# Performance work log

Hardware: AMD Instinct MI355X
Metric: run time of the kernel (lower is better)

## Reference

```python
import jax, jax.numpy as jnp
import numpy as np

BS, QS, H, NH, HD = 2, 2048, 1024, 16, 64


def setup_inputs() -> dict:
    key = jax.random.key(0)
    ks = jax.random.split(key, 10)
    s = 0.02
    x = jax.random.normal(ks[0], (BS, QS, H), jnp.float32)
    pos_emb = jax.random.normal(ks[1], (QS, H), jnp.float32)
    rr_bias = jax.random.normal(ks[2], (NH, HD), jnp.float32) * s
    rw_bias = jax.random.normal(ks[3], (NH, HD), jnp.float32) * s
    Wq = jax.random.normal(ks[4], (H, NH * HD), jnp.float32) * s
    Wk = jax.random.normal(ks[5], (H, NH * HD), jnp.float32) * s
    Wv = jax.random.normal(ks[6], (H, NH * HD), jnp.float32) * s
    Wr = jax.random.normal(ks[7], (H, NH * HD), jnp.float32) * s
    Wo = jax.random.normal(ks[8], (NH * HD, H), jnp.float32) * s
    ln_gamma = jnp.ones((H,), jnp.float32)
    ln_beta = jnp.zeros((H,), jnp.float32)
    # True = masked (filled with -inf); strict causal mask, ms = ks - qs = 0
    mask = jnp.triu(jnp.ones((QS, QS), bool), 1)
    return {"x": x, "mask": mask, "pos_emb": pos_emb, "rr_bias": rr_bias,
            "rw_bias": rw_bias, "Wq": Wq, "Wk": Wk, "Wv": Wv, "Wr": Wr,
            "Wo": Wo, "ln_gamma": ln_gamma, "ln_beta": ln_beta}


def _left_shift(x, bs):
    # x: [bs, qs, ks, n_head] -- Transformer-XL relative-shift trick
    b, qs, ksz, nh = x.shape
    pad = jnp.zeros((b, qs, 1, nh), x.dtype)
    xp = jnp.concatenate([pad, x], axis=2).reshape(b, ksz + 1, qs, nh)
    x = xp[:, 1:].reshape(b, qs, ksz, nh)
    # NOTE: original code uses diagonal offset (ks - bs) with bs = batch size
    tri = jnp.tril(jnp.ones((qs, ksz), x.dtype), ksz - bs)
    return x * tri[None, :, :, None]


def reference(x, mask, pos_emb, rr_bias, rw_bias, Wq, Wk, Wv, Wr, Wo, ln_gamma, ln_beta):
    bs, qs, hid = x.shape
    nh, dh = rr_bias.shape
    ksz = qs  # self-attention, no memory
    scale = 1.0 / dh ** 0.5
    q = (x @ Wq).reshape(bs, qs, nh, dh)
    k = (x @ Wk).reshape(bs, ksz, nh, dh)
    v = (x @ Wv).reshape(bs, ksz, nh, dh)
    r = (pos_emb @ Wr).reshape(qs, nh, dh)
    AC = jnp.einsum('bqnd,bknd->bqkn', q + rw_bias[None, None], k)
    BD = jnp.einsum('bqnd,knd->bqkn', q + rr_bias[None, None], r)
    BD = _left_shift(BD, bs)
    score = (AC + BD) * scale
    score = jnp.where(mask[None, :, :, None], -jnp.inf, score)
    prob = jax.nn.softmax(score, axis=2)  # softmax over key axis
    att = jnp.einsum('bqkn,bknd->bqnd', prob, v)
    out = att.reshape(bs, qs, nh * dh) @ Wo
    out = x + out  # residual (post-lnorm variant)
    mu = out.mean(-1, keepdims=True)
    var = ((out - mu) ** 2).mean(-1, keepdims=True)
    return (out - mu) / jnp.sqrt(var + 1e-5) * ln_gamma + ln_beta
```

## Files before the change

### kernel.cpp

```cpp
#include <hip/hip_runtime.h>
#include <hip/hip_bf16.h>


typedef _Float16 f16;
typedef __attribute__((ext_vector_type(8))) _Float16 f16x8;
typedef __attribute__((ext_vector_type(4))) float f32x4;

__device__ __forceinline__ void gload16(const f16* g, f16* l) {
  __builtin_amdgcn_global_load_lds((__attribute__((address_space(1))) void*)(g),
                                   (__attribute__((address_space(3))) void*)(l), 16, 0, 0);
}

__global__ __launch_bounds__(256) void cast2_kernel(const float* __restrict__ a,
                                                    f16* __restrict__ ao, int na4,
                                                    const float* __restrict__ b,
                                                    f16* __restrict__ bo, int nb4) {
  int i = blockIdx.x * 256 + threadIdx.x;
  const float* src;
  f16* dst;
  int j;
  if (i < na4) { src = a; dst = ao; j = i; }
  else { j = i - na4; if (j >= nb4) return; src = b; dst = bo; }
  f32x4 v = *(const f32x4*)&src[j * 4];
  f16 o0 = (f16)v[0], o1 = (f16)v[1], o2 = (f16)v[2], o3 = (f16)v[3];
  f16* p = &dst[j * 4];
  p[0] = o0; p[1] = o1; p[2] = o2; p[3] = o3;
}

__global__ __launch_bounds__(256) void wtrans5_kernel(
    const float* __restrict__ W0, const float* __restrict__ W1, const float* __restrict__ W2,
    const float* __restrict__ W3, const float* __restrict__ W4,
    f16* __restrict__ T0, f16* __restrict__ T1, f16* __restrict__ T2,
    f16* __restrict__ T3, f16* __restrict__ T4) {
  __shared__ float tile[32][33];
  const float* W;
  f16* WT;
  switch (blockIdx.z) {
    case 0: W = W0; WT = T0; break;
    case 1: W = W1; WT = T1; break;
    case 2: W = W2; WT = T2; break;
    case 3: W = W3; WT = T3; break;
    default: W = W4; WT = T4; break;
  }
  int k0 = blockIdx.x * 32, n0 = blockIdx.y * 32;
  int tx = threadIdx.x, ty = threadIdx.y;
#pragma unroll
  for (int i = 0; i < 4; ++i)
    tile[ty + i * 8][tx] = W[(size_t)(k0 + ty + i * 8) * 1024 + n0 + tx];
  __syncthreads();
#pragma unroll
  for (int i = 0; i < 4; ++i)
    WT[(size_t)(n0 + ty + i * 8) * 1024 + k0 + tx] = (f16)tile[tx][ty + i * 8];
}

__global__ __launch_bounds__(256) void gemm_qkv(
    const f16* __restrict__ A, const f16* __restrict__ Bq, const f16* __restrict__ Bk,
    const f16* __restrict__ Bv, f16* __restrict__ Qw, f16* __restrict__ Qr,
    f16* __restrict__ Kb, f16* __restrict__ VTb,
    const float* __restrict__ rw, const float* __restrict__ rr) {
  __shared__ f16 sm[17408];
  f16* As = sm;
  f16* Bs = sm + 8192;
  const int bsel = blockIdx.x >> 3;
  const f16* Bw = bsel == 0 ? Bq : (bsel == 1 ? Bk : Bv);
  const int n0 = (blockIdx.x & 7) * 128, m0 = blockIdx.y * 128;
  const int tid = threadIdx.x, lane = tid & 63, wv = tid >> 6;
  const int wm = wv >> 1, wn = wv & 1, lg = lane >> 4, ln = lane & 15;
  const int srow = lane >> 3, scol = (lane & 7) * 8;
  f32x4 acc[4][4] = {};

  for (int kt = 0; kt < 16; ++kt) {
    __syncthreads();
#pragma unroll
    for (int i = 0; i < 4; ++i) {
      int c = wv * 4 + i;
      gload16(A + (size_t)(m0 + c * 8 + srow) * 1024 + kt * 64 + scol, &As[c * 512]);
      gload16(Bw + (size_t)(n0 + c * 8 + srow) * 1024 + kt * 64 + scol, &Bs[c * 512]);
    }
    __syncthreads();
#pragma unroll
    for (int ks = 0; ks < 2; ++ks) {
      f16x8 af[4], bfr[4];
#pragma unroll
      for (int mi = 0; mi < 4; ++mi)
        af[mi] = *(const f16x8*)&As[(wm * 64 + mi * 16 + ln) * 64 + ks * 32 + 8 * lg];
#pragma unroll
      for (int ni = 0; ni < 4; ++ni)
        bfr[ni] = *(const f16x8*)&Bs[(wn * 64 + ni * 16 + ln) * 64 + ks * 32 + 8 * lg];
#pragma unroll
      for (int mi = 0; mi < 4; ++mi)
#pragma unroll
        for (int ni = 0; ni < 4; ++ni)
          acc[mi][ni] = __builtin_amdgcn_mfma_f32_16x16x32_f16(af[mi], bfr[ni],
                                                               acc[mi][ni], 0, 0, 0);
    }
  }

  if (bsel == 2) {
    __syncthreads();
    f16* T = sm;
#pragma unroll
    for (int mi = 0; mi < 4; ++mi)
#pragma unroll
      for (int ni = 0; ni < 4; ++ni)
#pragma unroll
        for (int r = 0; r < 4; ++r) {
          int ml = wm * 64 + mi * 16 + 4 * lg + r;
          int cl = wn * 64 + ni * 16 + ln;
          T[cl * 136 + ml] = (f16)acc[mi][ni][r];
        }
    __syncthreads();
    int cl = tid >> 1, mb = (tid & 1) * 64;
    int gc = n0 + cl, gm = m0 + mb;
    int hh = gc >> 6, dd = gc & 63, bb = gm >> 11, ss = gm & 2047;
    f16* dst = VTb + ((size_t)(bb * 16 + hh) * 64 + dd) * 2048 + ss;
    const f16* srcT = &T[cl * 136 + mb];
#pragma unroll
    for (int i = 0; i < 8; ++i) *(f16x8*)&dst[i * 8] = *(const f16x8*)&srcT[i * 8];
  } else {
#pragma unroll
    for (int mi = 0; mi < 4; ++mi)
#pragma unroll
      for (int ni = 0; ni < 4; ++ni)
#pragma unroll
        for (int r = 0; r < 4; ++r) {
          int m = m0 + wm * 64 + mi * 16 + 4 * lg + r;
          int c = n0 + wn * 64 + ni * 16 + ln;
          float v = acc[mi][ni][r];
          size_t off = (size_t)m * 1024 + c;
          if (bsel == 0) {
            Qw[off] = (f16)(v + rw[c]);
            Qr[off] = (f16)(v + rr[c]);
          } else {
            Kb[off] = (f16)v;
          }
        }
  }
}

template <int MODE>
__global__ __launch_bounds__(256) void gemm64(
    const f16* __restrict__ A, const f16* __restrict__ Bw,
    f16* __restrict__ out0, float* __restrict__ fout, const float* __restrict__ xres) {
  __shared__ f16 As[4096];
  __shared__ f16 Bs[8192];
  const int tid = threadIdx.x, lane = tid & 63, wv = tid >> 6;
  const int wm = wv >> 1, wn = wv & 1, lg = lane >> 4, ln = lane & 15;
  const int m0 = blockIdx.y * 64, n0 = blockIdx.x * 128;
  const int srow = lane >> 3, scol = (lane & 7) * 8;
  f32x4 acc[2][4] = {};

  for (int kt = 0; kt < 16; ++kt) {
    __syncthreads();
#pragma unroll
    for (int i = 0; i < 2; ++i) {
      int c = wv * 2 + i;
      gload16(A + (size_t)(m0 + c * 8 + srow) * 1024 + kt * 64 + scol, &As[c * 512]);
    }
#pragma unroll
    for (int i = 0; i < 4; ++i) {
      int c = wv * 4 + i;
      gload16(Bw + (size_t)(n0 + c * 8 + srow) * 1024 + kt * 64 + scol, &Bs[c * 512]);
    }
    __syncthreads();
#pragma unroll
    for (int ks = 0; ks < 2; ++ks) {
      f16x8 af[2], bfr[4];
#pragma unroll
      for (int mi = 0; mi < 2; ++mi)
        af[mi] = *(const f16x8*)&As[(wm * 32 + mi * 16 + ln) * 64 + ks * 32 + 8 * lg];
#pragma unroll
      for (int ni = 0; ni < 4; ++ni)
        bfr[ni] = *(const f16x8*)&Bs[(wn * 64 + ni * 16 + ln) * 64 + ks * 32 + 8 * lg];
#pragma unroll
      for (int mi = 0; mi < 2; ++mi)
#pragma unroll
        for (int ni = 0; ni < 4; ++ni)
          acc[mi][ni] = __builtin_amdgcn_mfma_f32_16x16x32_f16(af[mi], bfr[ni],
                                                               acc[mi][ni], 0, 0, 0);
    }
  }
#pragma unroll
  for (int mi = 0; mi < 2; ++mi)
#pragma unroll
    for (int ni = 0; ni < 4; ++ni)
#pragma unroll
      for (int r = 0; r < 4; ++r) {
        int m = m0 + wm * 32 + mi * 16 + 4 * lg + r;
        int c = n0 + wn * 64 + ni * 16 + ln;
        size_t off = (size_t)m * 1024 + c;
        if (MODE == 3) out0[off] = (f16)acc[mi][ni][r];
        else fout[off] = acc[mi][ni][r] + xres[off];
      }
}

__device__ __forceinline__ void chunk_map(int c, int& qt, int& ci) {
  if (c < 8) { qt = c; ci = 0; }
  else if (c < 24) { qt = 8 + ((c - 8) >> 1); ci = (c - 8) & 1; }
  else if (c < 48) { int d = c - 24; qt = 16 + d / 3; ci = d % 3; }
  else { int d = c - 48; qt = 24 + (d >> 2); ci = d & 3; }
}

__global__ __launch_bounds__(256) void attn_chunk(
    const f16* __restrict__ Qw, const f16* __restrict__ Qr,
    const f16* __restrict__ Kb, const f16* __restrict__ VT,
    const f16* __restrict__ Rb, f16* __restrict__ attb,
    f16* __restrict__ Opart, float* __restrict__ Mlp) {
  constexpr int LD = 72;
  constexpr int MW = 72;
  __shared__ f16 Kl[64 * LD];
  __shared__ f16 Vl[64 * LD];
  __shared__ f16 Rl[128 * LD];
  __shared__ f16 Sl[64 * MW];

  int qt, ci;
  chunk_map(blockIdx.x, qt, ci);
  const int h = blockIdx.y, b = blockIdx.z;
  const int q0 = qt * 64;
  const int kts = ci * 8;
  const int kte = min(kts + 7, qt);
  const int tid = threadIdx.x, lane = tid & 63, wv = tid >> 6;
  const int lg = lane >> 4, ln = lane & 15;

  const size_t qoff = ((size_t)(b * 2048 + q0 + wv * 16 + ln) * 16 + h) * 64 + 8 * lg;
  f16x8 aqw[2], aqr[2];
  aqw[0] = *(const f16x8*)&Qw[qoff];
  aqw[1] = *(const f16x8*)&Qw[qoff + 32];
  aqr[0] = *(const f16x8*)&Qr[qoff];
  aqr[1] = *(const f16x8*)&Qr[qoff + 32];

  f32x4 oacc[4] = {};
  float mrun[4] = {-1e30f, -1e30f, -1e30f, -1e30f};
  float lrun[4] = {0.f, 0.f, 0.f, 0.f};

  const int r4 = tid >> 2, c16 = (tid & 3) * 16;
  const int r2 = tid >> 1, c32 = (tid & 1) * 32;
  const int t0 = 48 - 16 * wv;

  f16x8 pk[2], pv[2], pr[4];
  auto load_regs = [&](int kt) {
    const int k0 = kt * 64;
    const f16* ksrc = Kb + ((size_t)(b * 2048 + k0 + r4) * 16 + h) * 64 + c16;
    pk[0] = *(const f16x8*)&ksrc[0];
    pk[1] = *(const f16x8*)&ksrc[8];
    const f16* vsrc = VT + ((size_t)(b * 16 + h) * 64 + r4) * 2048 + k0 + c16;
    pv[0] = *(const f16x8*)&vsrc[0];
    pv[1] = *(const f16x8*)&vsrc[8];
    const int j = 1984 - q0 + k0 + r2;
    if (j < 2048) {
      const f16* rsrc = Rb + ((size_t)j * 16 + h) * 64 + c32;
#pragma unroll
      for (int i = 0; i < 4; ++i) pr[i] = *(const f16x8*)&rsrc[i * 8];
    } else {
      f16x8 z = {};
#pragma unroll
      for (int i = 0; i < 4; ++i) pr[i] = z;
    }
  };
  auto write_lds = [&]() {
    *(f16x8*)&Kl[r4 * LD + c16] = pk[0];
    *(f16x8*)&Kl[r4 * LD + c16 + 8] = pk[1];
    *(f16x8*)&Vl[r4 * LD + c16] = pv[0];
    *(f16x8*)&Vl[r4 * LD + c16 + 8] = pv[1];
#pragma unroll
    for (int i = 0; i < 4; ++i) *(f16x8*)&Rl[r2 * LD + c32 + i * 8] = pr[i];
  };

  load_regs(kts);
  write_lds();
  __syncthreads();

  for (int kt = kts; kt <= kte; ++kt) {
    const int k0 = kt * 64;
    if (kt < kte) load_regs(kt + 1);

    f32x4 sc[4] = {};
#pragma unroll
    for (int ks = 0; ks < 2; ++ks)
#pragma unroll
      for (int ni = 0; ni < 4; ++ni) {
        f16x8 kf = *(const f16x8*)&Kl[(ni * 16 + ln) * LD + ks * 32 + 8 * lg];
        sc[ni] = __builtin_amdgcn_mfma_f32_16x16x32_f16(aqw[ks], kf, sc[ni], 0, 0, 0);
      }

    f32x4 mw[5] = {};
#pragma unroll
    for (int ks = 0; ks < 2; ++ks)
#pragma unroll
      for (int nj = 0; nj < 5; ++nj) {
        f16x8 rf = *(const f16x8*)&Rl[(t0 + nj * 16 + ln) * LD + ks * 32 + 8 * lg];
        mw[nj] = __builtin_amdgcn_mfma_f32_16x16x32_f16(aqr[ks], rf, mw[nj], 0, 0, 0);
      }

#pragma unroll
    for (int ni = 0; ni < 4; ++ni)
#pragma unroll
      for (int r = 0; r < 4; ++r) {
        const int s = 15 - 4 * lg - r;
        const int src = (ln + s) & 15;
        float v0 = __shfl(mw[ni][r], src, 16);
        float v1 = __shfl(mw[ni + 1][r], src, 16);
        float bd = (ln + s < 16) ? v0 : v1;
        float sv = (sc[ni][r] + bd) * 0.125f;
        int ql = 4 * lg + r, ki = ni * 16 + ln;
        if (k0 + ki > q0 + wv * 16 + ql) sv = -1e30f;
        sc[ni][r] = sv;
      }

#pragma unroll
    for (int r = 0; r < 4; ++r) {
      float mx = sc[0][r];
#pragma unroll
      for (int ni = 1; ni < 4; ++ni) mx = fmaxf(mx, sc[ni][r]);
#pragma unroll
      for (int off = 1; off < 16; off <<= 1) mx = fmaxf(mx, __shfl_xor(mx, off, 16));
      float mnew = fmaxf(mrun[r], mx);
      float corr = __expf(mrun[r] - mnew);
      mrun[r] = mnew;
      float rs = 0.f;
#pragma unroll
      for (int ni = 0; ni < 4; ++ni) {
        float p = __expf(sc[ni][r] - mnew);
        sc[ni][r] = p;
        rs += p;
      }
#pragma unroll
      for (int off = 1; off < 16; off <<= 1) rs += __shfl_xor(rs, off, 16);
      lrun[r] = lrun[r] * corr + rs;
#pragma unroll
      for (int ni = 0; ni < 4; ++ni) oacc[ni][r] *= corr;
    }

#pragma unroll
    for (int ni = 0; ni < 4; ++ni)
#pragma unroll
      for (int r = 0; r < 4; ++r)
        Sl[(wv * 16 + 4 * lg + r) * MW + ni * 16 + ln] = (f16)sc[ni][r];

#pragma unroll
    for (int ks = 0; ks < 2; ++ks) {
      f16x8 pf = *(const f16x8*)&Sl[(wv * 16 + ln) * MW + ks * 32 + 8 * lg];
#pragma unroll
      for (int ni = 0; ni < 4; ++ni) {
        f16x8 vf = *(const f16x8*)&Vl[(ni * 16 + ln) * LD + ks * 32 + 8 * lg];
        oacc[ni] = __builtin_amdgcn_mfma_f32_16x16x32_f16(pf, vf, oacc[ni], 0, 0, 0);
      }
    }

    __syncthreads();
    if (kt < kte) {
      write_lds();
      __syncthreads();
    }
  }

  if (qt < 8) {
#pragma unroll
    for (int ni = 0; ni < 4; ++ni)
#pragma unroll
      for (int r = 0; r < 4; ++r)
        Sl[(wv * 16 + 4 * lg + r) * MW + ni * 16 + ln] = (f16)(oacc[ni][r] / lrun[r]);
#pragma unroll
    for (int i = 0; i < 2; ++i) {
      int row = wv * 16 + i * 8 + (lane >> 3);
      int col = (lane & 7) * 8;
      *(f16x8*)&attb[((size_t)(b * 2048 + q0 + row) * 16 + h) * 64 + col] =
          *(const f16x8*)&Sl[row * MW + col];
    }
  } else {
    const size_t pidx = (size_t)(b * 16 + h) * 80 + blockIdx.x;
#pragma unroll
    for (int ni = 0; ni < 4; ++ni)
#pragma unroll
      for (int r = 0; r < 4; ++r)
        Sl[(wv * 16 + 4 * lg + r) * MW + ni * 16 + ln] = (f16)oacc[ni][r];
    if (ln == 0) {
#pragma unroll
      for (int r = 0; r < 4; ++r) {
        int row = wv * 16 + 4 * lg + r;
        Mlp[pidx * 128 + row] = mrun[r];
        Mlp[pidx * 128 + 64 + row] = lrun[r];
      }
    }
#pragma unroll
    for (int i = 0; i < 2; ++i) {
      int row = wv * 16 + i * 8 + (lane >> 3);
      int col = (lane & 7) * 8;
      *(f16x8*)&Opart[pidx * 4096 + row * 64 + col] = *(const f16x8*)&Sl[row * MW + col];
    }
  }
}

__global__ __launch_bounds__(256) void combine_kernel(
    const f16* __restrict__ Opart, const float* __restrict__ Mlp,
    f16* __restrict__ attb) {
  const int qt = 8 + blockIdx.x, h = blockIdx.y, b = blockIdx.z;
  const int nc = (qt + 8) >> 3;
  int cbase;
  if (qt < 16) cbase = 8 + 2 * (qt - 8);
  else if (qt < 24) cbase = 24 + 3 * (qt - 16);
  else cbase = 48 + 4 * (qt - 24);
  const int tid = threadIdx.x;
  const int row = tid >> 2, d0 = (tid & 3) * 16;
  const size_t pbase = (size_t)(b * 16 + h) * 80 + cbase;

  float m[4], l[4], w[4];
  float M = -1e30f;
#pragma unroll
  for (int i = 0; i < 4; ++i)
    if (i < nc) {
      m[i] = Mlp[(pbase + i) * 128 + row];
      l[i] = Mlp[(pbase + i) * 128 + 64 + row];
      M = fmaxf(M, m[i]);
    }
  float wsum = 0.f;
#pragma unroll
  for (int i = 0; i < 4; ++i)
    if (i < nc) {
      w[i] = __expf(m[i] - M);
      wsum += w[i] * l[i];
    }
  float o[16] = {};
#pragma unroll
  for (int i = 0; i < 4; ++i)
    if (i < nc) {
      const f16* src = &Opart[(pbase + i) * 4096 + row * 64 + d0];
      f16x8 v0 = *(const f16x8*)&src[0];
      f16x8 v1 = *(const f16x8*)&src[8];
#pragma unroll
      for (int j = 0; j < 8; ++j) {
        o[j] += w[i] * (float)v0[j];
        o[8 + j] += w[i] * (float)v1[j];
      }
    }
  float inv = 1.f / wsum;
  f16x8 r0, r1;
#pragma unroll
  for (int j = 0; j < 8; ++j) {
    r0[j] = (f16)(o[j] * inv);
    r1[j] = (f16)(o[8 + j] * inv);
  }
  f16* dst = &attb[((size_t)(b * 2048 + qt * 64 + row) * 16 + h) * 64 + d0];
  *(f16x8*)&dst[0] = r0;
  *(f16x8*)&dst[8] = r1;
}

__global__ __launch_bounds__(256) void ln_kernel(const float* __restrict__ pre,
                                                 const float* __restrict__ gamma,
                                                 const float* __restrict__ beta,
                                                 float* __restrict__ out) {
  __shared__ float red[8];
  const int row = blockIdx.x, t = threadIdx.x;
  f32x4 v = *(const f32x4*)&pre[(size_t)row * 1024 + t * 4];
  float s = v[0] + v[1] + v[2] + v[3];
  float s2 = v[0] * v[0] + v[1] * v[1] + v[2] * v[2] + v[3] * v[3];
#pragma unroll
  for (int off = 1; off < 64; off <<= 1) {
    s += __shfl_xor(s, off, 64);
    s2 += __shfl_xor(s2, off, 64);
  }
  if ((t & 63) == 0) {
    red[t >> 6] = s;
    red[(t >> 6) + 4] = s2;
  }
  __syncthreads();
  s = red[0] + red[1] + red[2] + red[3];
  s2 = red[4] + red[5] + red[6] + red[7];
  float mean = s * (1.f / 1024.f);
  float var = s2 * (1.f / 1024.f) - mean * mean;
  float rcp = rsqrtf(var + 1e-5f);
  f32x4 g = *(const f32x4*)&gamma[t * 4];
  f32x4 be = *(const f32x4*)&beta[t * 4];
  f32x4 o;
#pragma unroll
  for (int j = 0; j < 4; ++j) o[j] = (v[j] - mean) * rcp * g[j] + be[j];
  *(f32x4*)&out[(size_t)row * 1024 + t * 4] = o;
}

extern "C" void kernel_launch(void* const* d_in, const int* in_sizes, int n_in,
                              void* d_out, int out_size, void* d_ws, size_t ws_size,
                              hipStream_t stream) {
  const float* x = (const float*)d_in[0];
  const float* pe = (const float*)d_in[2];
  const float* rr = (const float*)d_in[3];
  const float* rw = (const float*)d_in[4];
  const float* Wq = (const float*)d_in[5];
  const float* Wk = (const float*)d_in[6];
  const float* Wv = (const float*)d_in[7];
  const float* Wr = (const float*)d_in[8];
  const float* Wo = (const float*)d_in[9];
  const float* gamma = (const float*)d_in[10];
  const float* beta = (const float*)d_in[11];
  float* out = (float*)d_out;

  char* w = (char*)d_ws;
  auto alloc = [&](size_t bytes) {
    char* p = w;
    w += (bytes + 255) & ~(size_t)255;
    return p;
  };
  float* preln = (float*)alloc(4096ull * 1024 * 4);
  f16* xb = (f16*)alloc(4096ull * 1024 * 2);
  f16* pb = (f16*)alloc(2048ull * 1024 * 2);
  f16* WTq = (f16*)alloc(1024ull * 1024 * 2);
  f16* WTk = (f16*)alloc(1024ull * 1024 * 2);
  f16* WTv = (f16*)alloc(1024ull * 1024 * 2);
  f16* WTr = (f16*)alloc(1024ull * 1024 * 2);
  f16* WTo = (f16*)alloc(1024ull * 1024 * 2);
  f16* Qw = (f16*)alloc(4096ull * 1024 * 2);
  f16* Qr = (f16*)alloc(4096ull * 1024 * 2);
  f16* Kb = (f16*)alloc(4096ull * 1024 * 2);
  f16* VTb = (f16*)alloc(4096ull * 1024 * 2);
  f16* Rb = (f16*)alloc(2048ull * 1024 * 2);
  f16* attb = (f16*)alloc(4096ull * 1024 * 2);
  f16* Opart = (f16*)alloc(2ull * 16 * 80 * 4096 * 2);
  float* Mlp = (float*)alloc(2ull * 16 * 80 * 128 * 4);

  cast2_kernel<<<6144, 256, 0, stream>>>(x, xb, 4096 * 1024 / 4, pe, pb, 2048 * 1024 / 4);
  wtrans5_kernel<<<dim3(32, 32, 5), dim3(32, 8), 0, stream>>>(Wq, Wk, Wv, Wr, Wo,
                                                              WTq, WTk, WTv, WTr, WTo);

  gemm_qkv<<<dim3(24, 32), 256, 0, stream>>>(xb, WTq, WTk, WTv, Qw, Qr, Kb, VTb, rw, rr);
  gemm64<3><<<dim3(8, 32), 256, 0, stream>>>(pb, WTr, Rb, nullptr, nullptr);

  attn_chunk<<<dim3(80, 16, 2), 256, 0, stream>>>(Qw, Qr, Kb, VTb, Rb, attb, Opart, Mlp);
  combine_kernel<<<dim3(24, 16, 2), 256, 0, stream>>>(Opart, Mlp, attb);

  gemm64<4><<<dim3(8, 64), 256, 0, stream>>>(attb, WTo, nullptr, preln, x);
  ln_kernel<<<4096, 256, 0, stream>>>(preln, gamma, beta, out);
}
```

Before: 348.3 us.

## Swizzle GEMM LDS tiles and ring-buffer R tiles with LDS-based relative shift

The GEMM kernels now XOR-swizzle the 16-byte chunk index when staging A/B tiles into LDS and when reading MFMA fragments, to avoid LDS bank conflicts on the strided fragment reads. The attention kernel keeps R in a 128-row ring buffer, so each key tile loads only 64 new R rows instead of reloading all 128. The relative-shift is now done by writing the BD tile to LDS (with a wider padded stride) and reading it back with a skewed index, replacing the per-element shuffles. This trades cross-lane shuffles and duplicate global loads for extra LDS writes and reads, and it also rounds the BD values to f16 before they are added to the scores, which loses some precision.

```diff
diff --git a/kernel.cpp b/kernel.cpp
--- a/kernel.cpp
+++ b/kernel.cpp
@@ -66,7 +66,8 @@
   const int n0 = (blockIdx.x & 7) * 128, m0 = blockIdx.y * 128;
   const int tid = threadIdx.x, lane = tid & 63, wv = tid >> 6;
   const int wm = wv >> 1, wn = wv & 1, lg = lane >> 4, ln = lane & 15;
-  const int srow = lane >> 3, scol = (lane & 7) * 8;
+  const int srow = lane >> 3;
+  const int sw = (lane & 7) ^ srow;
   f32x4 acc[4][4] = {};
 
   for (int kt = 0; kt < 16; ++kt) {
@@ -74,8 +75,8 @@
 #pragma unroll
     for (int i = 0; i < 4; ++i) {
       int c = wv * 4 + i;
-      gload16(A + (size_t)(m0 + c * 8 + srow) * 1024 + kt * 64 + scol, &As[c * 512]);
-      gload16(Bw + (size_t)(n0 + c * 8 + srow) * 1024 + kt * 64 + scol, &Bs[c * 512]);
+      gload16(A + (size_t)(m0 + c * 8 + srow) * 1024 + kt * 64 + sw * 8, &As[c * 512]);
+      gload16(Bw + (size_t)(n0 + c * 8 + srow) * 1024 + kt * 64 + sw * 8, &Bs[c * 512]);
     }
     __syncthreads();
 #pragma unroll
@@ -83,10 +84,12 @@
       f16x8 af[4], bfr[4];
 #pragma unroll
       for (int mi = 0; mi < 4; ++mi)
-        af[mi] = *(const f16x8*)&As[(wm * 64 + mi * 16 + ln) * 64 + ks * 32 + 8 * lg];
+        af[mi] = *(const f16x8*)&As[(wm * 64 + mi * 16 + ln) * 64 +
+                                    (((ks * 4 + lg) ^ (ln & 7)) * 8)];
 #pragma unroll
       for (int ni = 0; ni < 4; ++ni)
-        bfr[ni] = *(const f16x8*)&Bs[(wn * 64 + ni * 16 + ln) * 64 + ks * 32 + 8 * lg];
+        bfr[ni] = *(const f16x8*)&Bs[(wn * 64 + ni * 16 + ln) * 64 +
+                                     (((ks * 4 + lg) ^ (ln & 7)) * 8)];
 #pragma unroll
       for (int mi = 0; mi < 4; ++mi)
 #pragma unroll
@@ -147,7 +150,8 @@
   const int tid = threadIdx.x, lane = tid & 63, wv = tid >> 6;
   const int wm = wv >> 1, wn = wv & 1, lg = lane >> 4, ln = lane & 15;
   const int m0 = blockIdx.y * 64, n0 = blockIdx.x * 128;
-  const int srow = lane >> 3, scol = (lane & 7) * 8;
+  const int srow = lane >> 3;
+  const int sw = (lane & 7) ^ srow;
   f32x4 acc[2][4] = {};
 
   for (int kt = 0; kt < 16; ++kt) {
@@ -155,12 +159,12 @@
 #pragma unroll
     for (int i = 0; i < 2; ++i) {
       int c = wv * 2 + i;
-      gload16(A + (size_t)(m0 + c * 8 + srow) * 1024 + kt * 64 + scol, &As[c * 512]);
+      gload16(A + (size_t)(m0 + c * 8 + srow) * 1024 + kt * 64 + sw * 8, &As[c * 512]);
     }
 #pragma unroll
     for (int i = 0; i < 4; ++i) {
       int c = wv * 4 + i;
-      gload16(Bw + (size_t)(n0 + c * 8 + srow) * 1024 + kt * 64 + scol, &Bs[c * 512]);
+      gload16(Bw + (size_t)(n0 + c * 8 + srow) * 1024 + kt * 64 + sw * 8, &Bs[c * 512]);
     }
     __syncthreads();
 #pragma unroll
@@ -168,10 +172,12 @@
       f16x8 af[2], bfr[4];
 #pragma unroll
       for (int mi = 0; mi < 2; ++mi)
-        af[mi] = *(const f16x8*)&As[(wm * 32 + mi * 16 + ln) * 64 + ks * 32 + 8 * lg];
+        af[mi] = *(const f16x8*)&As[(wm * 32 + mi * 16 + ln) * 64 +
+                                    (((ks * 4 + lg) ^ (ln & 7)) * 8)];
 #pragma unroll
       for (int ni = 0; ni < 4; ++ni)
-        bfr[ni] = *(const f16x8*)&Bs[(wn * 64 + ni * 16 + ln) * 64 + ks * 32 + 8 * lg];
+        bfr[ni] = *(const f16x8*)&Bs[(wn * 64 + ni * 16 + ln) * 64 +
+                                     (((ks * 4 + lg) ^ (ln & 7)) * 8)];
 #pragma unroll
       for (int mi = 0; mi < 2; ++mi)
 #pragma unroll
@@ -207,7 +213,7 @@
     const f16* __restrict__ Rb, f16* __restrict__ attb,
     f16* __restrict__ Opart, float* __restrict__ Mlp) {
   constexpr int LD = 72;
-  constexpr int MW = 72;
+  constexpr int MW = 88;
   __shared__ f16 Kl[64 * LD];
   __shared__ f16 Vl[64 * LD];
   __shared__ f16 Rl[128 * LD];
@@ -234,11 +240,10 @@
   float lrun[4] = {0.f, 0.f, 0.f, 0.f};
 
   const int r4 = tid >> 2, c16 = (tid & 3) * 16;
-  const int r2 = tid >> 1, c32 = (tid & 1) * 32;
   const int t0 = 48 - 16 * wv;
 
-  f16x8 pk[2], pv[2], pr[4];
-  auto load_regs = [&](int kt) {
+  f16x8 pk[2], pv[2], prn[2];
+  auto load_kv = [&](int kt) {
     const int k0 = kt * 64;
     const f16* ksrc = Kb + ((size_t)(b * 2048 + k0 + r4) * 16 + h) * 64 + c16;
     pk[0] = *(const f16x8*)&ksrc[0];
@@ -246,33 +251,58 @@
     const f16* vsrc = VT + ((size_t)(b * 16 + h) * 64 + r4) * 2048 + k0 + c16;
     pv[0] = *(const f16x8*)&vsrc[0];
     pv[1] = *(const f16x8*)&vsrc[8];
-    const int j = 1984 - q0 + k0 + r2;
+  };
+  auto load_r = [&](int jbcur) {
+    const int j = jbcur + 128 + r4;
     if (j < 2048) {
-      const f16* rsrc = Rb + ((size_t)j * 16 + h) * 64 + c32;
-#pragma unroll
-      for (int i = 0; i < 4; ++i) pr[i] = *(const f16x8*)&rsrc[i * 8];
+      const f16* rsrc = Rb + ((size_t)j * 16 + h) * 64 + c16;
+      prn[0] = *(const f16x8*)&rsrc[0];
+      prn[1] = *(const f16x8*)&rsrc[8];
     } else {
       f16x8 z = {};
-#pragma unroll
-      for (int i = 0; i < 4; ++i) pr[i] = z;
+      prn[0] = z;
+      prn[1] = z;
     }
   };
-  auto write_lds = [&]() {
+  auto write_kv = [&]() {
     *(f16x8*)&Kl[r4 * LD + c16] = pk[0];
     *(f16x8*)&Kl[r4 * LD + c16 + 8] = pk[1];
     *(f16x8*)&Vl[r4 * LD + c16] = pv[0];
     *(f16x8*)&Vl[r4 * LD + c16 + 8] = pv[1];
-#pragma unroll
-    for (int i = 0; i < 4; ++i) *(f16x8*)&Rl[r2 * LD + c32 + i * 8] = pr[i];
   };
-
-  load_regs(kts);
-  write_lds();
+  auto write_r = [&](int jbcur) {
+    const int slot = (jbcur + r4) & 127;
+    *(f16x8*)&Rl[slot * LD + c16] = prn[0];
+    *(f16x8*)&Rl[slot * LD + c16 + 8] = prn[1];
+  };
+
+  const int jb0 = 1984 - q0 + kts * 64;
+  load_kv(kts);
+  write_kv();
+  {
+    const int r2 = tid >> 1, c32 = (tid & 1) * 32;
+    const int j = jb0 + r2;
+    const int slot = j & 127;
+    if (j < 2048) {
+      const f16* rsrc = Rb + ((size_t)j * 16 + h) * 64 + c32;
+#pragma unroll
+      for (int i = 0; i < 4; ++i)
+        *(f16x8*)&Rl[slot * LD + c32 + i * 8] = *(const f16x8*)&rsrc[i * 8];
+    } else {
+      f16x8 z = {};
+#pragma unroll
+      for (int i = 0; i < 4; ++i) *(f16x8*)&Rl[slot * LD + c32 + i * 8] = z;
+    }
+  }
   __syncthreads();
 
   for (int kt = kts; kt <= kte; ++kt) {
     const int k0 = kt * 64;
-    if (kt < kte) load_regs(kt + 1);
+    const int jb = 1984 - q0 + k0;
+    if (kt < kte) {
+      load_kv(kt + 1);
+      load_r(jb);
+    }
 
     f32x4 sc[4] = {};
 #pragma unroll
@@ -288,23 +318,27 @@
     for (int ks = 0; ks < 2; ++ks)
 #pragma unroll
       for (int nj = 0; nj < 5; ++nj) {
-        f16x8 rf = *(const f16x8*)&Rl[(t0 + nj * 16 + ln) * LD + ks * 32 + 8 * lg];
+        const int slot = (jb + t0 + nj * 16 + ln) & 127;
+        f16x8 rf = *(const f16x8*)&Rl[slot * LD + ks * 32 + 8 * lg];
         mw[nj] = __builtin_amdgcn_mfma_f32_16x16x32_f16(aqr[ks], rf, mw[nj], 0, 0, 0);
       }
 
 #pragma unroll
+    for (int nj = 0; nj < 5; ++nj)
+#pragma unroll
+      for (int r = 0; r < 4; ++r)
+        Sl[(wv * 16 + 4 * lg + r) * MW + nj * 16 + ln] = (f16)mw[nj][r];
+
+#pragma unroll
     for (int ni = 0; ni < 4; ++ni)
 #pragma unroll
       for (int r = 0; r < 4; ++r) {
-        const int s = 15 - 4 * lg - r;
-        const int src = (ln + s) & 15;
-        float v0 = __shfl(mw[ni][r], src, 16);
-        float v1 = __shfl(mw[ni + 1][r], src, 16);
-        float bd = (ln + s < 16) ? v0 : v1;
-        float sv = (sc[ni][r] + bd) * 0.125f;
-        int ql = 4 * lg + r, ki = ni * 16 + ln;
-        if (k0 + ki > q0 + wv * 16 + ql) sv = -1e30f;
-        sc[ni][r] = sv;
+        int ql = 4 * lg + r;
+        int ki = ni * 16 + ln;
+        float bd = (float)Sl[(wv * 16 + ql) * MW + ki - ql + 15];
+        float s = (sc[ni][r] + bd) * 0.125f;
+        if (k0 + ki > q0 + wv * 16 + ql) s = -1e30f;
+        sc[ni][r] = s;
       }
 
 #pragma unroll
@@ -349,7 +383,8 @@
 
     __syncthreads();
     if (kt < kte) {
-      write_lds();
+      write_kv();
+      write_r(jb);
       __syncthreads();
     }
   }
```

Result: faster. 320.1 us (-8.1%).
